# Kernel optimization log

Hardware: AMD Instinct MI355X
Metric: run time of the kernel (lower is better)

Reference implementation:

```python
import jax, jax.numpy as jnp
import numpy as np

T_TOK, N_UNITS, E, H, L_PATH, N_PATHS, B, VOCAB = 16, 4096, 128, 128, 32, 1024, 8, 16384
MAX_PATH_LEN = 32
PAD_ID = 0


def _run_lstm(x, Wi, Wh, b):
    # x: [T, N, E]; torch gate order i, f, g, o
    Hh = Wh.shape[1]
    h0 = jnp.zeros((x.shape[1], Hh), x.dtype)
    def step(carry, xt):
        h, c = carry
        g = xt @ Wi.T + h @ Wh.T + b
        i, f, gg, o = jnp.split(g, 4, axis=-1)
        c = jax.nn.sigmoid(f) * c + jax.nn.sigmoid(i) * jnp.tanh(gg)
        h = jax.nn.sigmoid(o) * jnp.tanh(c)
        return (h, c), h
    _, ys = jax.lax.scan(step, (h0, h0), x)
    return ys


def _bilstm(x, lengths, Wif, Whf, bf, Wib, Whb, bb):
    # emulates pack_padded_sequence + bidirectional LSTM + pad_packed (zeros past length)
    T = x.shape[0]
    t = jnp.arange(T)[:, None]
    valid = t < lengths[None, :]
    out_f = _run_lstm(x, Wif, Whf, bf)
    rev = jnp.clip(lengths[None, :] - 1 - t, 0, T - 1)  # reverse within each valid prefix
    x_rev = jnp.take_along_axis(x, rev[:, :, None], axis=0)
    out_b = jnp.take_along_axis(_run_lstm(x_rev, Wib, Whb, bb), rev[:, :, None], axis=0)
    return jnp.concatenate([out_f, out_b], axis=-1) * valid[:, :, None]


def _layernorm(x, g, b):
    m = x.mean(-1, keepdims=True)
    v = ((x - m) ** 2).mean(-1, keepdims=True)
    return (x - m) * jax.lax.rsqrt(v + 1e-5) * g + b


def _forward(units, paths, unit_per_data, path_per_data, emb, tl_Wif, tl_Whf, tl_bf,
             tl_Wib, tl_Whb, tl_bb, lin_W, lin_b, ln_g, ln_b, attn_w, attn_b,
             pl_Wif, pl_Whf, pl_bf, pl_Wib, pl_Whb, pl_bb, ul_W, ul_b):
    # ---- _token_encoder ----
    is_pad = units == PAD_ID
    tok_len = jnp.where(is_pad.any(0), jnp.argmax(is_pad, 0), units.shape[0])
    x = emb[units]                                              # [T, NU, E]
    h = _bilstm(x, tok_len, tl_Wif, tl_Whf, tl_bf, tl_Wib, tl_Whb, tl_bb)  # [T, NU, 2H]
    out = h @ lin_W.T + lin_b                                   # [T, NU, E]
    q = jnp.tanh(_layernorm(out, ln_g, ln_b))
    scores = q @ attn_w.T + attn_b                              # [T, NU, 1] local attention
    scores = jnp.where(is_pad[:, :, None], -1e9, scores)
    w = jax.nn.softmax(scores, axis=0)
    tok_feat = jnp.einsum('tn,tne->ne', w[..., 0], out)         # [NU, E]
    # ---- _unit_to_path (vectorized ragged gather) ----
    Lp, Pn = paths.shape
    has_end = (paths == -1).any(0)
    fe = jnp.where(has_end, jnp.argmax(paths == -1, 0), Lp)
    ML = min(Lp, MAX_PATH_LEN)
    nb = unit_per_data.shape[0]
    data_of_path = jnp.repeat(jnp.arange(nb), path_per_data, total_repeat_length=Pn)
    u_off = jnp.cumsum(unit_per_data) - unit_per_data
    off_p = u_off[data_of_path]
    un_p = unit_per_data[data_of_path]
    pL = paths[:ML]
    t = jnp.arange(ML)[:, None]
    within = t < fe[None, :]
    keep = within & (pL >= 0) & (pL < un_p[None, :])
    gidx = jnp.clip(jnp.clip(pL, 0, None) + off_p[None, :], 0, tok_feat.shape[0] - 1)
    feats = tok_feat[gidx] * keep[:, :, None]                   # [ML, P, E]
    mask = jnp.where(within, (pL < 0) | (pL > un_p[None, :]), True)
    # ---- _path_encoder ----
    p_len = jnp.where(mask.any(0), jnp.argmax(mask, 0), ML)
    hp = _bilstm(feats, p_len, pl_Wif, pl_Whf, pl_bf, pl_Wib, pl_Whb, pl_bb)
    return hp @ ul_W.T + ul_b                                   # [ML, P, E]


def setup_inputs() -> dict:
    rng = np.random.default_rng(0)
    tok_len = rng.integers(4, T_TOK + 1, N_UNITS); tok_len[0] = T_TOK
    units = rng.integers(1, VOCAB, (T_TOK, N_UNITS))
    units = np.where(np.arange(T_TOK)[:, None] < tok_len[None, :], units, PAD_ID)
    upd = N_UNITS // B
    p_len = rng.integers(8, L_PATH + 1, N_PATHS); p_len[0] = L_PATH
    paths = rng.integers(0, upd, (L_PATH, N_PATHS))
    paths = np.where(np.arange(L_PATH)[:, None] < p_len[None, :], paths, -1)
    key = jax.random.key(0)
    ks = iter(jax.random.split(key, 24))
    def pn(shape, s=0.08):
        return (jax.random.normal(next(ks), shape) * s).astype(jnp.float32)
    return dict(
        units=jnp.asarray(units, jnp.int32),
        paths=jnp.asarray(paths, jnp.int32),
        unit_per_data=jnp.full((B,), upd, jnp.int32),
        path_per_data=jnp.full((B,), N_PATHS // B, jnp.int32),
        emb=pn((VOCAB, E)),
        tl_Wif=pn((4 * H, E)), tl_Whf=pn((4 * H, H)), tl_bf=pn((4 * H,)),
        tl_Wib=pn((4 * H, E)), tl_Whb=pn((4 * H, H)), tl_bb=pn((4 * H,)),
        lin_W=pn((E, 2 * H)), lin_b=pn((E,)),
        ln_g=jnp.ones((E,), jnp.float32), ln_b=jnp.zeros((E,), jnp.float32),
        attn_w=pn((1, E)), attn_b=pn((1,)),
        pl_Wif=pn((4 * H, E)), pl_Whf=pn((4 * H, H)), pl_bf=pn((4 * H,)),
        pl_Wib=pn((4 * H, E)), pl_Whb=pn((4 * H, H)), pl_bb=pn((4 * H,)),
        ul_W=pn((E, 2 * H)), ul_b=pn((E,)),
    )


def reference(units, paths, unit_per_data, path_per_data, emb, tl_Wif, tl_Whf, tl_bf,
              tl_Wib, tl_Whb, tl_bb, lin_W, lin_b, ln_g, ln_b, attn_w, attn_b,
              pl_Wif, pl_Whf, pl_bf, pl_Wib, pl_Whb, pl_bb, ul_W, ul_b):
    return _forward(units, paths, unit_per_data, path_per_data, emb, tl_Wif, tl_Whf, tl_bf,
                    tl_Wib, tl_Whb, tl_bb, lin_W, lin_b, ln_g, ln_b, attn_w, attn_b,
                    pl_Wif, pl_Whf, pl_bf, pl_Wib, pl_Whb, pl_bb, ul_W, ul_b)
```

## Files before the change

### kernel.cpp

```cpp
#include <hip/hip_runtime.h>
#include <cstdint>
#include <cstddef>

#define T_TOKN 16
#define NUNITS 4096
#define LPATH  32
#define NPATHS 1024
#define BNUM   8

typedef __attribute__((ext_vector_type(8))) short short8;
typedef __attribute__((ext_vector_type(4))) short short4x;
typedef __attribute__((ext_vector_type(4))) float f32x4;

enum : size_t {
  OFF_WFRAG   = 0,
  OFF_LINFRAG = 262144,
  OFF_OUTF    = 294912,
  OFF_OUTB    = OFF_OUTF + 4194304,
  OFF_OUTLIN  = OFF_OUTB + 4194304,
  OFF_SCORES  = OFF_OUTLIN + 8388608,
  OFF_TOKFEAT = OFF_SCORES + 65536,
  OFF_POUTF   = OFF_TOKFEAT + 524288,
  OFF_POUTB   = OFF_POUTF + 2097152,
  OFF_INT     = OFF_POUTB + 2097152,
  WS_FLOATS   = OFF_INT + 8192
};

static __device__ __forceinline__ unsigned short f2bf(float f) {
  union { float f; unsigned u; } v; v.f = f;
  unsigned r = v.u + 0x7fffu + ((v.u >> 16) & 1u);
  return (unsigned short)(r >> 16);
}
static __device__ __forceinline__ float sigf(float x)      { return 1.f / (1.f + __expf(-x)); }
static __device__ __forceinline__ float tanhfast(float x)  { return 2.f / (1.f + __expf(-2.f * x)) - 1.f; }

__global__ void prep_kernel(
    const float* __restrict__ tWif, const float* __restrict__ tWhf,
    const float* __restrict__ tWib, const float* __restrict__ tWhb,
    const float* __restrict__ pWif, const float* __restrict__ pWhf,
    const float* __restrict__ pWib, const float* __restrict__ pWhb,
    const float* __restrict__ linW, const float* __restrict__ ulW,
    float* __restrict__ ws)
{
  int idx = blockIdx.x * 256 + threadIdx.x;
  if (idx < 524288) {
    unsigned short* wf = (unsigned short*)(ws + OFF_WFRAG);
    int mat = idx >> 17, rem = idx & 131071;
    int i  = rem & 7;
    int lane = (rem >> 3) & 63;
    int ct = (rem >> 9) & 3;
    int ks = (rem >> 11) & 7;
    int wv = (rem >> 14) & 7;
    int g = wv * 64 + ct * 16 + (lane & 15);
    int k = ks * 32 + ((lane >> 4) << 3) + i;
    const float* Wi; const float* Wh;
    switch (mat) {
      case 0: Wi = tWif; Wh = tWhf; break;
      case 1: Wi = tWib; Wh = tWhb; break;
      case 2: Wi = pWif; Wh = pWhf; break;
      default: Wi = pWib; Wh = pWhb; break;
    }
    float v = (k < 128) ? Wi[g * 128 + k] : Wh[g * 128 + (k - 128)];
    wf[idx] = f2bf(v);
  } else if (idx < 524288 + 65536) {
    unsigned short* lf = (unsigned short*)(ws + OFF_LINFRAG);
    int i2 = idx - 524288;
    int mat = i2 >> 15, rem = i2 & 32767;
    int i  = rem & 7;
    int lane = (rem >> 3) & 63;
    int ks = (rem >> 9) & 7;
    int ct = (rem >> 12) & 7;
    int e = ct * 16 + (lane & 15);
    int k = ks * 32 + ((lane >> 4) << 3) + i;
    const float* W = mat ? ulW : linW;
    lf[i2] = f2bf(W[e * 256 + k]);
  }
}

__global__ void len_kernel(const int* __restrict__ units, const int* __restrict__ paths,
                           const int* __restrict__ upd, const int* __restrict__ ppd,
                           int* __restrict__ ip)
{
  int idx = blockIdx.x * 256 + threadIdx.x;
  int* tok_len = ip;
  int* fe_a    = ip + 4096;
  int* p_len   = ip + 5120;
  int* off_p   = ip + 6144;
  int* un_p    = ip + 7168;
  if (idx < 4096) {
    int len = T_TOKN;
    for (int t = 0; t < T_TOKN; ++t)
      if (units[t * NUNITS + idx] == 0) { len = t; break; }
    tok_len[idx] = len;
  } else if (idx < 5120) {
    int p = idx - 4096;
    int cum = 0; int d = BNUM - 1;
    for (int dd = 0; dd < BNUM; ++dd) {
      int c2 = cum + ppd[dd];
      if (p < c2) { d = dd; break; }
      cum = c2;
    }
    int off = 0;
    for (int dd = 0; dd < d; ++dd) off += upd[dd];
    int un = upd[d];
    off_p[p] = off; un_p[p] = un;
    int f = LPATH;
    for (int t = 0; t < LPATH; ++t)
      if (paths[t * NPATHS + p] == -1) { f = t; break; }
    fe_a[p] = f;
    int pl = LPATH;
    for (int t = 0; t < LPATH; ++t) {
      int v = paths[t * NPATHS + p];
      if ((t >= f) || (v < 0) || (v > un)) { pl = t; break; }
    }
    p_len[p] = pl;
  }
}

template <int MODE>
__global__ __launch_bounds__(1024, 4) void lstm_kernel(
    const unsigned short* __restrict__ wfragAll,
    const float* __restrict__ biasF, const float* __restrict__ biasB,
    const float* __restrict__ src,
    const int* __restrict__ idxsrc,
    const int* __restrict__ lens,
    const int* __restrict__ fe_a, const int* __restrict__ off_p, const int* __restrict__ un_p,
    unsigned short* __restrict__ outF, unsigned short* __restrict__ outB)
{
  constexpr int NN   = MODE ? NPATHS : NUNITS;
  constexpr int TT   = MODE ? LPATH : T_TOKN;
  constexpr int M    = MODE ? 8 : 32;
  constexpr int MR   = MODE ? 16 : 32;
  constexpr int NRT  = MR / 16;
  constexpr int ASTR = 264;
  constexpr int GSTR = 514;
  constexpr int NU   = MODE ? 1 : 4;

  __shared__ unsigned short ash[MR * ASTR];
  __shared__ float gates[MR * GSTR];

  int tid  = threadIdx.x;
  int dir  = blockIdx.y;
  int n0   = blockIdx.x * M;
  int lane = tid & 63, wv = tid >> 6;

  const unsigned short* wbase =
      wfragAll + (size_t)((MODE ? 2 : 0) + dir) * 131072;
  int wv8 = wv >> 1;
  short8 bfr[8][2];
#pragma unroll
  for (int ks = 0; ks < 8; ++ks)
#pragma unroll
    for (int c2 = 0; c2 < 2; ++c2) {
      int ct = ((wv & 1) << 1) | c2;
      bfr[ks][c2] = *(const short8*)&wbase[((((wv8 * 8 + ks) * 4 + ct) * 64) + lane) * 8];
    }

  if (MODE == 0) {
    for (int i = tid; i < MR * 128; i += 1024)
      ash[(i >> 7) * ASTR + 128 + (i & 127)] = 0;
  } else {
    for (int i = tid; i < MR * ASTR; i += 1024) ash[i] = 0;
  }
  __syncthreads();

  int jj = tid & 127, ug = tid >> 7;
  const float* bcp = dir ? biasB : biasF;
  float b4[4];
#pragma unroll
  for (int q = 0; q < 4; ++q) b4[q] = bcp[q * 128 + jj];
  float cst[NU];
  int   ulen[NU];
#pragma unroll
  for (int i = 0; i < NU; ++i) {
    cst[i] = 0.f;
    int u = ug * NU + i;
    ulen[i] = lens[n0 + u];
  }

  int gu, gk0;
  if (MODE == 0) { gu = tid >> 5; gk0 = (tid & 31) * 4; }
  else           { gu = tid >> 7; gk0 = tid & 127; }
  int glen = lens[n0 + gu];
  int gfe = 0, goff = 0, gun = 0;
  if (MODE) { gfe = fe_a[n0 + gu]; goff = off_p[n0 + gu]; gun = un_p[n0 + gu]; }

  for (int t = 0; t < TT; ++t) {
    if (MODE == 0) {
      int tau = dir ? min(max(glen - 1 - t, 0), TT - 1) : t;
      int tok = idxsrc[tau * NN + (n0 + gu)];
      float4 v = *(const float4*)&src[(size_t)tok * 128 + gk0];
      short4x x4;
      x4[0] = (short)f2bf(v.x); x4[1] = (short)f2bf(v.y);
      x4[2] = (short)f2bf(v.z); x4[3] = (short)f2bf(v.w);
      *(short4x*)&ash[gu * ASTR + gk0] = x4;
    } else {
      int tau = dir ? min(max(glen - 1 - t, 0), TT - 1) : t;
      int v = idxsrc[tau * NN + (n0 + gu)];
      bool keep = (tau < gfe) && (v >= 0) && (v < gun);
      float x0 = 0.f;
      if (keep) {
        int gi = min(v + goff, NUNITS - 1);
        x0 = src[(size_t)gi * 128 + gk0];
      }
      ash[gu * ASTR + gk0] = f2bf(x0);
    }
    __syncthreads();

    f32x4 acc[NRT][2];
#pragma unroll
    for (int rt = 0; rt < NRT; ++rt)
#pragma unroll
      for (int c2 = 0; c2 < 2; ++c2) {
        f32x4 z = {0.f, 0.f, 0.f, 0.f};
        acc[rt][c2] = z;
      }
#pragma unroll
    for (int ks = 0; ks < 8; ++ks) {
      short8 afr[NRT];
#pragma unroll
      for (int rt = 0; rt < NRT; ++rt)
        afr[rt] = *(const short8*)&ash[(rt * 16 + (lane & 15)) * ASTR + ks * 32 + ((lane >> 4) << 3)];
#pragma unroll
      for (int rt = 0; rt < NRT; ++rt)
#pragma unroll
        for (int c2 = 0; c2 < 2; ++c2)
          acc[rt][c2] = __builtin_amdgcn_mfma_f32_16x16x32_bf16(
              afr[rt], bfr[ks][c2], acc[rt][c2], 0, 0, 0);
    }
#pragma unroll
    for (int rt = 0; rt < NRT; ++rt)
#pragma unroll
      for (int c2 = 0; c2 < 2; ++c2) {
        int g = wv * 32 + c2 * 16 + (lane & 15);
#pragma unroll
        for (int r = 0; r < 4; ++r) {
          int u = rt * 16 + ((lane >> 4) << 2) + r;
          gates[u * GSTR + g] = acc[rt][c2][r];
        }
      }
    __syncthreads();

#pragma unroll
    for (int i = 0; i < NU; ++i) {
      int u = ug * NU + i;
      int n = n0 + u;
      float p0 = gates[u * GSTR + jj]       + b4[0];
      float p1 = gates[u * GSTR + 128 + jj] + b4[1];
      float p2 = gates[u * GSTR + 256 + jj] + b4[2];
      float p3 = gates[u * GSTR + 384 + jj] + b4[3];
      float ig = sigf(p0), fg = sigf(p1), gg = tanhfast(p2), og = sigf(p3);
      float c = fg * cst[i] + ig * gg;
      cst[i] = c;
      float h = og * tanhfast(c);
      unsigned short hb = f2bf(h);
      ash[u * ASTR + 128 + jj] = hb;
      if (dir == 0) {
        outF[((size_t)t * NN + n) * 128 + jj] = hb;
      } else {
        int L = ulen[i];
        if (t < L) outB[((size_t)(L - 1 - t) * NN + n) * 128 + jj] = hb;
        else       outB[((size_t)t * NN + n) * 128 + jj] = 0;
      }
    }
  }
}

template <int EPI>
__global__ __launch_bounds__(256) void gemm_mfma(
    const unsigned short* __restrict__ INf, const unsigned short* __restrict__ INb,
    const int* __restrict__ lens,
    const unsigned short* __restrict__ Bfrag, const float* __restrict__ bias,
    float* __restrict__ OUT, float* __restrict__ scores,
    const float* __restrict__ lng, const float* __restrict__ lnb,
    const float* __restrict__ attw, const float* __restrict__ attb,
    const int* __restrict__ units, int Nn)
{
  constexpr int OSTR = 132;
  __shared__ float outs[64 * OSTR];
  __shared__ float red1[256];
  __shared__ float red2[256];
  __shared__ float rowm[64], rowr[64];
  __shared__ float awsh[128], lgsh[128], lbsh[128];

  int tid = threadIdx.x, lane = tid & 63, wv = tid >> 6;
  int row0 = blockIdx.x * 64;
  int t = row0 / Nn, n0 = row0 % Nn;

  if (EPI == 1 && tid < 128) {
    awsh[tid] = attw[tid]; lgsh[tid] = lng[tid]; lbsh[tid] = lnb[tid];
  }

  short8 bfr[8][2];
#pragma unroll
  for (int ks = 0; ks < 8; ++ks)
#pragma unroll
    for (int c2 = 0; c2 < 2; ++c2) {
      int ct = wv * 2 + c2;
      bfr[ks][c2] = *(const short8*)&Bfrag[(((ct * 8 + ks) * 64) + lane) * 8];
    }

  int rb = lane & 15;
  int koq = (lane >> 4) << 3;
  bool val[4];
#pragma unroll
  for (int rt = 0; rt < 4; ++rt)
    val[rt] = (EPI == 1) ? true : (t < lens[n0 + rt * 16 + rb]);

  f32x4 acc[4][2];
#pragma unroll
  for (int rt = 0; rt < 4; ++rt)
#pragma unroll
    for (int c2 = 0; c2 < 2; ++c2) {
      f32x4 z = {0.f, 0.f, 0.f, 0.f};
      acc[rt][c2] = z;
    }

#pragma unroll
  for (int ks = 0; ks < 8; ++ks) {
    const unsigned short* P = (ks < 4) ? INf : INb;
    int koff = (ks & 3) * 32 + koq;
#pragma unroll
    for (int rt = 0; rt < 4; ++rt) {
      short8 a = {0, 0, 0, 0, 0, 0, 0, 0};
      if (val[rt])
        a = *(const short8*)&P[((size_t)(row0 + rt * 16 + rb)) * 128 + koff];
#pragma unroll
      for (int c2 = 0; c2 < 2; ++c2)
        acc[rt][c2] = __builtin_amdgcn_mfma_f32_16x16x32_bf16(
            a, bfr[ks][c2], acc[rt][c2], 0, 0, 0);
    }
  }

  float bc[2];
#pragma unroll
  for (int c2 = 0; c2 < 2; ++c2) bc[c2] = bias[wv * 32 + c2 * 16 + rb];
#pragma unroll
  for (int rt = 0; rt < 4; ++rt)
#pragma unroll
    for (int c2 = 0; c2 < 2; ++c2) {
      int col = wv * 32 + c2 * 16 + rb;
      int ub  = rt * 16 + ((lane >> 4) << 2);
#pragma unroll
      for (int r = 0; r < 4; ++r)
        outs[(ub + r) * OSTR + col] = acc[rt][c2][r] + bc[c2];
    }
  __syncthreads();

  int row = tid >> 2, seg = tid & 3;
  const float* rp = &outs[row * OSTR + seg * 32];
  size_t go = ((size_t)(row0 + row)) * 128 + seg * 32;

  if (EPI == 0) {
#pragma unroll
    for (int x = 0; x < 8; ++x)
      *(f32x4*)&OUT[go + x * 4] = *(const f32x4*)&rp[x * 4];
  } else {
    f32x4 v[8];
    float s = 0.f, s2 = 0.f;
#pragma unroll
    for (int x = 0; x < 8; ++x) {
      v[x] = *(const f32x4*)&rp[x * 4];
#pragma unroll
      for (int c = 0; c < 4; ++c) { s += v[x][c]; s2 += v[x][c] * v[x][c]; }
    }
    red1[tid] = s; red2[tid] = s2;
    __syncthreads();
    if (tid < 64) {
      float a = red1[tid * 4] + red1[tid * 4 + 1] + red1[tid * 4 + 2] + red1[tid * 4 + 3];
      float b = red2[tid * 4] + red2[tid * 4 + 1] + red2[tid * 4 + 2] + red2[tid * 4 + 3];
      float m = a * (1.f / 128.f);
      float var = b * (1.f / 128.f) - m * m;
      rowm[tid] = m;
      rowr[tid] = rsqrtf(var + 1e-5f);
    }
    __syncthreads();
    float m = rowm[row], rs = rowr[row];
    float sp = 0.f;
#pragma unroll
    for (int x = 0; x < 8; ++x) {
#pragma unroll
      for (int c = 0; c < 4; ++c) {
        int col = seg * 32 + x * 4 + c;
        float q = tanhfast((v[x][c] - m) * rs * lgsh[col] + lbsh[col]);
        sp += q * awsh[col];
      }
      *(f32x4*)&OUT[go + x * 4] = v[x];
    }
    red1[tid] = sp;
    __syncthreads();
    if (tid < 64) {
      float s3 = red1[tid * 4] + red1[tid * 4 + 1] + red1[tid * 4 + 2] + red1[tid * 4 + 3]
               + attb[0];
      int n = n0 + tid;
      if (units[t * NUNITS + n] == 0) s3 = -1e9f;
      scores[t * NUNITS + n] = s3;
    }
  }
}

__global__ __launch_bounds__(128) void softmax_feat_kernel(
    const float* __restrict__ scores, const float* __restrict__ out_lin,
    float* __restrict__ tok_feat)
{
  int n = blockIdx.x;
  int e = threadIdx.x;
  float s[T_TOKN];
  float m = -1e30f;
#pragma unroll
  for (int t = 0; t < T_TOKN; ++t) { s[t] = scores[t * NUNITS + n]; m = fmaxf(m, s[t]); }
  float sum = 0.f;
#pragma unroll
  for (int t = 0; t < T_TOKN; ++t) { s[t] = expf(s[t] - m); sum += s[t]; }
  float inv = 1.f / sum;
  float a = 0.f;
#pragma unroll
  for (int t = 0; t < T_TOKN; ++t)
    a += s[t] * inv * out_lin[((size_t)t * NUNITS + n) * 128 + e];
  tok_feat[n * 128 + e] = a;
}

extern "C" void kernel_launch(void* const* d_in, const int* in_sizes, int n_in,
                              void* d_out, int out_size, void* d_ws, size_t ws_size,
                              hipStream_t stream)
{
  const int*   units = (const int*)d_in[0];
  const int*   paths = (const int*)d_in[1];
  const int*   upd   = (const int*)d_in[2];
  const int*   ppd   = (const int*)d_in[3];
  const float* emb   = (const float*)d_in[4];
  const float* tWif  = (const float*)d_in[5];
  const float* tWhf  = (const float*)d_in[6];
  const float* tbf   = (const float*)d_in[7];
  const float* tWib  = (const float*)d_in[8];
  const float* tWhb  = (const float*)d_in[9];
  const float* tbb   = (const float*)d_in[10];
  const float* linW  = (const float*)d_in[11];
  const float* linb  = (const float*)d_in[12];
  const float* lng   = (const float*)d_in[13];
  const float* lnb   = (const float*)d_in[14];
  const float* attw  = (const float*)d_in[15];
  const float* attb  = (const float*)d_in[16];
  const float* pWif  = (const float*)d_in[17];
  const float* pWhf  = (const float*)d_in[18];
  const float* pbf   = (const float*)d_in[19];
  const float* pWib  = (const float*)d_in[20];
  const float* pWhb  = (const float*)d_in[21];
  const float* pbb   = (const float*)d_in[22];
  const float* ulW   = (const float*)d_in[23];
  const float* ulb   = (const float*)d_in[24];

  float* ws = (float*)d_ws;
  int*   ip = (int*)(ws + OFF_INT);
  if (ws_size < WS_FLOATS * sizeof(float)) return;

  unsigned short* wfrag   = (unsigned short*)(ws + OFF_WFRAG);
  unsigned short* linfrag = (unsigned short*)(ws + OFF_LINFRAG);
  unsigned short* ulfrag  = linfrag + 32768;
  unsigned short* OUTF  = (unsigned short*)(ws + OFF_OUTF);
  unsigned short* OUTB  = (unsigned short*)(ws + OFF_OUTB);
  unsigned short* POUTF = (unsigned short*)(ws + OFF_POUTF);
  unsigned short* POUTB = (unsigned short*)(ws + OFF_POUTB);

  prep_kernel<<<2304, 256, 0, stream>>>(tWif, tWhf, tWib, tWhb,
                                        pWif, pWhf, pWib, pWhb,
                                        linW, ulW, ws);
  len_kernel<<<20, 256, 0, stream>>>(units, paths, upd, ppd, ip);

  lstm_kernel<0><<<dim3(128, 2), 1024, 0, stream>>>(
      wfrag, tbf, tbb, emb, units, ip , nullptr, nullptr, nullptr,
      OUTF, OUTB);

  gemm_mfma<1><<<1024, 256, 0, stream>>>(
      OUTF, OUTB, ip , linfrag, linb,
      ws + OFF_OUTLIN, ws + OFF_SCORES, lng, lnb, attw, attb, units, NUNITS);

  softmax_feat_kernel<<<4096, 128, 0, stream>>>(ws + OFF_SCORES, ws + OFF_OUTLIN,
                                                ws + OFF_TOKFEAT);

  lstm_kernel<1><<<dim3(128, 2), 1024, 0, stream>>>(
      wfrag, pbf, pbb, ws + OFF_TOKFEAT, paths, ip + 5120 ,
      ip + 4096 , ip + 6144 , ip + 7168 ,
      POUTF, POUTB);

  gemm_mfma<0><<<512, 256, 0, stream>>>(
      POUTF, POUTB, ip + 5120 , ulfrag, ulb,
      (float*)d_out, nullptr, nullptr, nullptr, nullptr, nullptr, nullptr, NPATHS);
}
```

Before: 340.6 us.

## Prefetch next-step LSTM inputs during MFMA, vectorize gate math, merge length kernel

```diff
diff --git a/kernel.cpp b/kernel.cpp
--- a/kernel.cpp
+++ b/kernel.cpp
@@ -31,6 +31,9 @@
   unsigned r = v.u + 0x7fffu + ((v.u >> 16) & 1u);
   return (unsigned short)(r >> 16);
 }
+static __device__ __forceinline__ unsigned pack_bf(float a, float b) {
+  return (unsigned)f2bf(a) | ((unsigned)f2bf(b) << 16);
+}
 static __device__ __forceinline__ float sigf(float x)      { return 1.f / (1.f + __expf(-x)); }
 static __device__ __forceinline__ float tanhfast(float x)  { return 2.f / (1.f + __expf(-2.f * x)) - 1.f; }
 
@@ -40,7 +43,9 @@
     const float* __restrict__ pWif, const float* __restrict__ pWhf,
     const float* __restrict__ pWib, const float* __restrict__ pWhb,
     const float* __restrict__ linW, const float* __restrict__ ulW,
-    float* __restrict__ ws)
+    const int* __restrict__ units, const int* __restrict__ paths,
+    const int* __restrict__ upd, const int* __restrict__ ppd,
+    float* __restrict__ ws, int* __restrict__ ip)
 {
   int idx = blockIdx.x * 256 + threadIdx.x;
   if (idx < 524288) {
@@ -74,26 +79,18 @@
     int k = ks * 32 + ((lane >> 4) << 3) + i;
     const float* W = mat ? ulW : linW;
     lf[i2] = f2bf(W[e * 256 + k]);
-  }
-}
-
-__global__ void len_kernel(const int* __restrict__ units, const int* __restrict__ paths,
-                           const int* __restrict__ upd, const int* __restrict__ ppd,
-                           int* __restrict__ ip)
-{
-  int idx = blockIdx.x * 256 + threadIdx.x;
-  int* tok_len = ip;
-  int* fe_a    = ip + 4096;
-  int* p_len   = ip + 5120;
-  int* off_p   = ip + 6144;
-  int* un_p    = ip + 7168;
-  if (idx < 4096) {
+  } else if (idx < 589824 + 4096) {
+    int n = idx - 589824;
     int len = T_TOKN;
     for (int t = 0; t < T_TOKN; ++t)
-      if (units[t * NUNITS + idx] == 0) { len = t; break; }
-    tok_len[idx] = len;
-  } else if (idx < 5120) {
-    int p = idx - 4096;
+      if (units[t * NUNITS + n] == 0) { len = t; break; }
+    ip[n] = len;
+  } else if (idx < 589824 + 5120) {
+    int p = idx - (589824 + 4096);
+    int* fe_a  = ip + 4096;
+    int* p_len = ip + 5120;
+    int* off_p = ip + 6144;
+    int* un_p  = ip + 7168;
     int cum = 0; int d = BNUM - 1;
     for (int dd = 0; dd < BNUM; ++dd) {
       int c2 = cum + ppd[dd];
@@ -134,7 +131,6 @@
   constexpr int NRT  = MR / 16;
   constexpr int ASTR = 264;
   constexpr int GSTR = 514;
-  constexpr int NU   = MODE ? 1 : 4;
 
   __shared__ unsigned short ash[MR * ASTR];
   __shared__ float gates[MR * GSTR];
@@ -162,105 +158,149 @@
   } else {
     for (int i = tid; i < MR * ASTR; i += 1024) ash[i] = 0;
   }
-  __syncthreads();
-
-  int jj = tid & 127, ug = tid >> 7;
+
   const float* bcp = dir ? biasB : biasF;
-  float b4[4];
-#pragma unroll
-  for (int q = 0; q < 4; ++q) b4[q] = bcp[q * 128 + jj];
-  float cst[NU];
+  int j2 = MODE ? (tid & 127) : ((tid & 63) * 2);
+  int ug = MODE ? (tid >> 7)  : (tid >> 6);
+  float2 b2[4];
+#pragma unroll
+  for (int q = 0; q < 4; ++q) {
+    if (MODE == 0) b2[q] = *(const float2*)&bcp[q * 128 + j2];
+    else           b2[q] = make_float2(bcp[q * 128 + j2], 0.f);
+  }
+  constexpr int NU = MODE ? 1 : 2;
+  float cst0[NU], cst1[NU];
   int   ulen[NU];
 #pragma unroll
   for (int i = 0; i < NU; ++i) {
-    cst[i] = 0.f;
-    int u = ug * NU + i;
-    ulen[i] = lens[n0 + u];
+    cst0[i] = 0.f; cst1[i] = 0.f;
+    ulen[i] = lens[n0 + ug * NU + i];
   }
 
   int gu, gk0;
   if (MODE == 0) { gu = tid >> 5; gk0 = (tid & 31) * 4; }
   else           { gu = tid >> 7; gk0 = tid & 127; }
-  int glen = lens[n0 + gu];
+  int gn = n0 + gu;
+  int glen = lens[gn];
   int gfe = 0, goff = 0, gun = 0;
-  if (MODE) { gfe = fe_a[n0 + gu]; goff = off_p[n0 + gu]; gun = un_p[n0 + gu]; }
+  if (MODE) { gfe = fe_a[gn]; goff = off_p[gn]; gun = un_p[gn]; }
+
+  float4 xq; float xs;
+  if (MODE == 0) {
+    int tau = dir ? min(max(glen - 1, 0), TT - 1) : 0;
+    int tok = idxsrc[tau * NN + gn];
+    xq = *(const float4*)&src[(size_t)tok * 128 + gk0];
+  } else {
+    int tau = dir ? min(max(glen - 1, 0), TT - 1) : 0;
+    int v = idxsrc[tau * NN + gn];
+    bool keep = (tau < gfe) && (v >= 0) && (v < gun);
+    xs = 0.f;
+    if (keep) xs = src[(size_t)min(v + goff, NUNITS - 1) * 128 + gk0];
+  }
+  __syncthreads();
 
   for (int t = 0; t < TT; ++t) {
     if (MODE == 0) {
-      int tau = dir ? min(max(glen - 1 - t, 0), TT - 1) : t;
-      int tok = idxsrc[tau * NN + (n0 + gu)];
-      float4 v = *(const float4*)&src[(size_t)tok * 128 + gk0];
       short4x x4;
-      x4[0] = (short)f2bf(v.x); x4[1] = (short)f2bf(v.y);
-      x4[2] = (short)f2bf(v.z); x4[3] = (short)f2bf(v.w);
+      x4[0] = (short)f2bf(xq.x); x4[1] = (short)f2bf(xq.y);
+      x4[2] = (short)f2bf(xq.z); x4[3] = (short)f2bf(xq.w);
       *(short4x*)&ash[gu * ASTR + gk0] = x4;
     } else {
-      int tau = dir ? min(max(glen - 1 - t, 0), TT - 1) : t;
-      int v = idxsrc[tau * NN + (n0 + gu)];
-      bool keep = (tau < gfe) && (v >= 0) && (v < gun);
-      float x0 = 0.f;
-      if (keep) {
-        int gi = min(v + goff, NUNITS - 1);
-        x0 = src[(size_t)gi * 128 + gk0];
+      ash[gu * ASTR + gk0] = f2bf(xs);
+    }
+    __syncthreads();
+
+    {
+      int tn = (t + 1 < TT) ? t + 1 : t;
+      int taun = dir ? min(max(glen - 1 - tn, 0), TT - 1) : tn;
+      int vn = idxsrc[taun * NN + gn];
+      f32x4 acc[NRT][2];
+#pragma unroll
+      for (int rt = 0; rt < NRT; ++rt)
+#pragma unroll
+        for (int c2 = 0; c2 < 2; ++c2) {
+          f32x4 z = {0.f, 0.f, 0.f, 0.f};
+          acc[rt][c2] = z;
+        }
+#pragma unroll
+      for (int ks = 0; ks < 8; ++ks) {
+        short8 afr[NRT];
+#pragma unroll
+        for (int rt = 0; rt < NRT; ++rt)
+          afr[rt] = *(const short8*)&ash[(rt * 16 + (lane & 15)) * ASTR + ks * 32 + ((lane >> 4) << 3)];
+#pragma unroll
+        for (int rt = 0; rt < NRT; ++rt)
+#pragma unroll
+          for (int c2 = 0; c2 < 2; ++c2)
+            acc[rt][c2] = __builtin_amdgcn_mfma_f32_16x16x32_bf16(
+                afr[rt], bfr[ks][c2], acc[rt][c2], 0, 0, 0);
       }
-      ash[gu * ASTR + gk0] = f2bf(x0);
-    }
-    __syncthreads();
-
-    f32x4 acc[NRT][2];
-#pragma unroll
-    for (int rt = 0; rt < NRT; ++rt)
-#pragma unroll
-      for (int c2 = 0; c2 < 2; ++c2) {
-        f32x4 z = {0.f, 0.f, 0.f, 0.f};
-        acc[rt][c2] = z;
+      if (MODE == 0) {
+        xq = *(const float4*)&src[(size_t)vn * 128 + gk0];
+      } else {
+        bool keep = (taun < gfe) && (vn >= 0) && (vn < gun);
+        xs = 0.f;
+        if (keep) xs = src[(size_t)min(vn + goff, NUNITS - 1) * 128 + gk0];
       }
 #pragma unroll
-    for (int ks = 0; ks < 8; ++ks) {
-      short8 afr[NRT];
-#pragma unroll
       for (int rt = 0; rt < NRT; ++rt)
-        afr[rt] = *(const short8*)&ash[(rt * 16 + (lane & 15)) * ASTR + ks * 32 + ((lane >> 4) << 3)];
-#pragma unroll
-      for (int rt = 0; rt < NRT; ++rt)
-#pragma unroll
-        for (int c2 = 0; c2 < 2; ++c2)
-          acc[rt][c2] = __builtin_amdgcn_mfma_f32_16x16x32_bf16(
-              afr[rt], bfr[ks][c2], acc[rt][c2], 0, 0, 0);
-    }
-#pragma unroll
-    for (int rt = 0; rt < NRT; ++rt)
-#pragma unroll
-      for (int c2 = 0; c2 < 2; ++c2) {
-        int g = wv * 32 + c2 * 16 + (lane & 15);
-#pragma unroll
-        for (int r = 0; r < 4; ++r) {
-          int u = rt * 16 + ((lane >> 4) << 2) + r;
-          gates[u * GSTR + g] = acc[rt][c2][r];
+#pragma unroll
+        for (int c2 = 0; c2 < 2; ++c2) {
+          int g = wv * 32 + c2 * 16 + (lane & 15);
+#pragma unroll
+          for (int r = 0; r < 4; ++r) {
+            int u = rt * 16 + ((lane >> 4) << 2) + r;
+            gates[u * GSTR + g] = acc[rt][c2][r];
+          }
         }
-      }
+    }
     __syncthreads();
 
 #pragma unroll
     for (int i = 0; i < NU; ++i) {
       int u = ug * NU + i;
       int n = n0 + u;
-      float p0 = gates[u * GSTR + jj]       + b4[0];
-      float p1 = gates[u * GSTR + 128 + jj] + b4[1];
-      float p2 = gates[u * GSTR + 256 + jj] + b4[2];
-      float p3 = gates[u * GSTR + 384 + jj] + b4[3];
-      float ig = sigf(p0), fg = sigf(p1), gg = tanhfast(p2), og = sigf(p3);
-      float c = fg * cst[i] + ig * gg;
-      cst[i] = c;
-      float h = og * tanhfast(c);
-      unsigned short hb = f2bf(h);
-      ash[u * ASTR + 128 + jj] = hb;
-      if (dir == 0) {
-        outF[((size_t)t * NN + n) * 128 + jj] = hb;
+      if (MODE == 0) {
+        float2 g0 = *(const float2*)&gates[u * GSTR + j2];
+        float2 g1 = *(const float2*)&gates[u * GSTR + 128 + j2];
+        float2 g2 = *(const float2*)&gates[u * GSTR + 256 + j2];
+        float2 g3 = *(const float2*)&gates[u * GSTR + 384 + j2];
+        float i0 = sigf(g0.x + b2[0].x), i1 = sigf(g0.y + b2[0].y);
+        float f0 = sigf(g1.x + b2[1].x), f1 = sigf(g1.y + b2[1].y);
+        float c0 = tanhfast(g2.x + b2[2].x), c1 = tanhfast(g2.y + b2[2].y);
+        float o0 = sigf(g3.x + b2[3].x), o1 = sigf(g3.y + b2[3].y);
+        float cA = f0 * cst0[i] + i0 * c0;
+        float cB = f1 * cst1[i] + i1 * c1;
+        cst0[i] = cA; cst1[i] = cB;
+        float h0 = o0 * tanhfast(cA);
+        float h1 = o1 * tanhfast(cB);
+        unsigned hp = pack_bf(h0, h1);
+        *(unsigned*)&ash[u * ASTR + 128 + j2] = hp;
+        if (dir == 0) {
+          *(unsigned*)&outF[((size_t)t * NN + n) * 128 + j2] = hp;
+        } else {
+          int L = ulen[i];
+          if (t < L) *(unsigned*)&outB[((size_t)(L - 1 - t) * NN + n) * 128 + j2] = hp;
+          else       *(unsigned*)&outB[((size_t)t * NN + n) * 128 + j2] = 0;
+        }
       } else {
-        int L = ulen[i];
-        if (t < L) outB[((size_t)(L - 1 - t) * NN + n) * 128 + jj] = hb;
-        else       outB[((size_t)t * NN + n) * 128 + jj] = 0;
+        float p0 = gates[u * GSTR + j2]       + b2[0].x;
+        float p1 = gates[u * GSTR + 128 + j2] + b2[1].x;
+        float p2 = gates[u * GSTR + 256 + j2] + b2[2].x;
+        float p3 = gates[u * GSTR + 384 + j2] + b2[3].x;
+        float ig = sigf(p0), fg = sigf(p1), gg = tanhfast(p2), og = sigf(p3);
+        float c = fg * cst0[i] + ig * gg;
+        cst0[i] = c;
+        float h = og * tanhfast(c);
+        unsigned short hb = f2bf(h);
+        ash[u * ASTR + 128 + j2] = hb;
+        if (dir == 0) {
+          outF[((size_t)t * NN + n) * 128 + j2] = hb;
+        } else {
+          int L = ulen[i];
+          if (t < L) outB[((size_t)(L - 1 - t) * NN + n) * 128 + j2] = hb;
+          else       outB[((size_t)t * NN + n) * 128 + j2] = 0;
+        }
       }
     }
   }
@@ -462,10 +502,10 @@
   unsigned short* POUTF = (unsigned short*)(ws + OFF_POUTF);
   unsigned short* POUTB = (unsigned short*)(ws + OFF_POUTB);
 
-  prep_kernel<<<2304, 256, 0, stream>>>(tWif, tWhf, tWib, tWhb,
+  prep_kernel<<<2324, 256, 0, stream>>>(tWif, tWhf, tWib, tWhb,
                                         pWif, pWhf, pWib, pWhb,
-                                        linW, ulW, ws);
-  len_kernel<<<20, 256, 0, stream>>>(units, paths, upd, ppd, ip);
+                                        linW, ulW, units, paths, upd, ppd,
+                                        ws, ip);
 
   lstm_kernel<0><<<dim3(128, 2), 1024, 0, stream>>>(
       wfrag, tbf, tbb, emb, units, ip , nullptr, nullptr, nullptr,
```

New measurement: 320.7 us. 1.06x faster.
